# Optimization experiments

Measured on AMD Instinct MI355X. Metric: run time of the kernel, lower is better.

The kernel has to match this reference:

```python
import jax, jax.numpy as jnp
import numpy as np

N = 50000   # n_nodes (== input_dim, featureless identity features)
E = 800000  # edges per support (avg degree 16)
D = 200     # embed_dim (hardcoded in GIN)
C = 10      # num_classes


def setup_inputs() -> dict:
    key = jax.random.key(0)
    ks = jax.random.split(key, 8)
    x = jnp.zeros((N, 1), jnp.float32)  # unused: layer 0 is featureless
    rows0 = jax.random.randint(ks[0], (E,), 0, N, dtype=jnp.int32)
    cols0 = jax.random.randint(ks[1], (E,), 0, N, dtype=jnp.int32)
    vals0 = jax.random.uniform(ks[2], (E,), jnp.float32)
    rows1 = jax.random.randint(ks[3], (E,), 0, N, dtype=jnp.int32)
    cols1 = jax.random.randint(ks[4], (E,), 0, N, dtype=jnp.int32)
    vals1 = jax.random.uniform(ks[5], (E,), jnp.float32)
    W0 = jax.random.normal(ks[6], (N, D), jnp.float32) * 0.02
    W1 = jax.random.normal(ks[7], (D, C), jnp.float32) * 0.05
    eps0 = jnp.zeros((1,), jnp.float32)  # train_eps init (~1e-4 in repo)
    eps1 = jnp.zeros((1,), jnp.float32)
    return dict(x=x, rows0=rows0, cols0=cols0, vals0=vals0,
                rows1=rows1, cols1=cols1, vals1=vals1,
                W0=W0, W1=W1, eps0=eps0, eps1=eps1)


def reference(x, rows0, cols0, vals0, rows1, cols1, vals1, W0, W1, eps0, eps1):
    # sparse A @ X via gather + segment-sum (A in COO: rows, cols, vals)
    def spmm(r, c, v, X):
        return jax.ops.segment_sum(v[:, None] * X[c], r, num_segments=N)

    # Layer 0 (featureless, num_mlp_layers==1):
    #   AX = sum_i A_i ; out = AX @ W0 + 0.1*(1+eps0)*W0
    h0 = spmm(rows0, cols0, vals0, W0) + spmm(rows1, cols1, vals1, W0) \
         + 0.1 * (1.0 + eps0[0]) * W0
    h = jax.nn.relu(h0)  # [N, D]

    # Layer 1 (with features): out = (sum_i A_i @ h + 0.1*(1+eps1)*h) @ W1
    ax = spmm(rows0, cols0, vals0, h) + spmm(rows1, cols1, vals1, h)
    out = (ax + 0.1 * (1.0 + eps1[0]) * h) @ W1  # [N, C]
    return out
```

## Files before the change

### kernel.cpp

```cpp
#include <hip/hip_runtime.h>

#define N_NODES 50000
#define E_EDGES 800000
#define E2      (2 * E_EDGES)
#define D_DIM   200
#define C_CLS   10
#define NB_BUCKET 196
#define BATCH     4096
#define NB_SCATTER ((E2 + BATCH - 1) / BATCH)
#define NB_CONV    ((N_NODES * D_DIM / 4 + 255) / 256)
#define CAP       12288

static __device__ __forceinline__ unsigned f2bf(float f) {
    unsigned u = __float_as_uint(f);
    return (u + 0x7FFFu + ((u >> 16) & 1u)) >> 16;
}
static __device__ __forceinline__ float bf_lo(unsigned u) {
    return __uint_as_float(u << 16);
}
static __device__ __forceinline__ float bf_hi(unsigned u) {
    return __uint_as_float(u & 0xFFFF0000u);
}

__global__ __launch_bounds__(256) void convert_scatter_kernel(
        const float* __restrict__ W0, unsigned short* __restrict__ W0h,
        const int* __restrict__ rows0, const int* __restrict__ cols0,
        const float* __restrict__ vals0,
        const int* __restrict__ rows1, const int* __restrict__ cols1,
        const float* __restrict__ vals1,
        int* __restrict__ bcur,
        int2* __restrict__ stage) {
    __shared__ int cntL[NB_BUCKET];
    __shared__ int baseL[NB_BUCKET];
    __shared__ int offL[NB_BUCKET];
    __shared__ int2 recL[BATCH];

    if (blockIdx.x >= NB_SCATTER) {
        int i = ((blockIdx.x - NB_SCATTER) * 256 + threadIdx.x) * 4;
        if (i < N_NODES * D_DIM) {
            float4 f = *(const float4*)(W0 + i);
            uint2 p;
            p.x = f2bf(f.x) | (f2bf(f.y) << 16);
            p.y = f2bf(f.z) | (f2bf(f.w) << 16);
            *(uint2*)(W0h + i) = p;
        }
        return;
    }

    const int tid = threadIdx.x;
    const int e0 = blockIdx.x * BATCH;

    for (int b = tid; b < NB_BUCKET; b += 256) cntL[b] = 0;
    __syncthreads();

#pragma unroll
    for (int k = 0; k < BATCH / 256; ++k) {
        int idx = k * 256 + tid;
        int e = e0 + idx;
        if (e < E2) {
            int r, c;
            float v;
            if (e < E_EDGES) {
                r = rows0[e]; c = cols0[e]; v = vals0[e];
            } else {
                int e1 = e - E_EDGES;
                r = rows1[e1]; c = cols1[e1]; v = vals1[e1];
            }
            recL[idx] = make_int2((int)((unsigned)r | ((unsigned)c << 16)),
                                  __float_as_int(v));
            atomicAdd(&cntL[r >> 8], 1);
        }
    }
    __syncthreads();

    for (int b = tid; b < NB_BUCKET; b += 256) {
        int c = cntL[b];
        baseL[b] = (c > 0) ? atomicAdd(&bcur[b], c) : 0;
        offL[b] = 0;
    }
    __syncthreads();

#pragma unroll
    for (int k = 0; k < BATCH / 256; ++k) {
        int idx = k * 256 + tid;
        int e = e0 + idx;
        if (e < E2) {
            int2 rec = recL[idx];
            int b = (int)(((unsigned)rec.x & 0xFFFFu) >> 8);
            int pos = baseL[b] + atomicAdd(&offL[b], 1);
            stage[(size_t)b * CAP + pos] = rec;
        }
    }
}

__global__ __launch_bounds__(256) void build_csr_kernel(
        const int* __restrict__ bcur,
        const int2* __restrict__ stage,
        int* __restrict__ ticket,
        int2* __restrict__ rowseg,
        unsigned* __restrict__ cv4) {
    __shared__ int hist[256];
    __shared__ int lcur[256];
    __shared__ int ws4[4];
    __shared__ int sbase;
    const int b = blockIdx.x;
    const int tid = threadIdx.x;
    const int lane = tid & 63;
    const int w = tid >> 6;
    hist[tid] = 0;
    __syncthreads();

    const int n = bcur[b];
    const int2* __restrict__ sp = stage + (size_t)b * CAP;
    for (int i = tid; i < n; i += 256)
        atomicAdd(&hist[(unsigned)sp[i].x & 255u], 1);
    __syncthreads();

    int v = hist[tid];
    const int orig = v;
#pragma unroll
    for (int off = 1; off < 64; off <<= 1) {
        int t = __shfl_up(v, off, 64);
        if (lane >= off) v += t;
    }
    if (lane == 63) ws4[w] = v;
    __syncthreads();
    if (tid == 0) {
        int s = 0;
#pragma unroll
        for (int k = 0; k < 4; ++k) { int t = ws4[k]; ws4[k] = s; s += t; }
    }
    __syncthreads();
    v += ws4[w];

    if (tid == 255) sbase = atomicAdd(ticket, v);
    __syncthreads();

    const int start = sbase + v - orig;
    const int row = (b << 8) + tid;
    if (row < N_NODES) rowseg[row] = make_int2(start, orig);
    lcur[tid] = start;
    __syncthreads();

    for (int i = tid; i < n; i += 256) {
        int2 rec = sp[i];
        unsigned u = (unsigned)rec.x;
        int pos = atomicAdd(&lcur[u & 255u], 1);
        cv4[pos] = (u & 0xFFFF0000u) | f2bf(__int_as_float(rec.y));
    }
}

__global__ __launch_bounds__(256) void spmm_layer0_fused_kernel(
        const int2* __restrict__ rowseg,
        const unsigned* __restrict__ cv4,
        const unsigned short* __restrict__ W0h,
        const float* __restrict__ W1,
        const float* __restrict__ eps0,
        float* __restrict__ g) {
    __shared__ float W1s[D_DIM * C_CLS];
    for (int i = threadIdx.x; i < D_DIM * C_CLS; i += blockDim.x) W1s[i] = W1[i];
    __syncthreads();

    const int lane = threadIdx.x & 63;
    const int n = __builtin_amdgcn_readfirstlane(blockIdx.x * 4 + (threadIdx.x >> 6));
    if (n >= N_NODES) return;
    const float s0 = 0.1f * (1.0f + eps0[0]);
    const bool act = (lane < 50);
    const uint2* __restrict__ F = (const uint2*)W0h;

    const int2 seg = rowseg[n];
    const int beg  = seg.x;
    const int endp = seg.x + seg.y;
    float a0 = 0.f, a1 = 0.f, a2 = 0.f, a3 = 0.f;

    int e = beg;
    for (; e + 8 <= endp; e += 8) {
        unsigned w0 = cv4[e],     w1 = cv4[e + 1], w2 = cv4[e + 2], w3 = cv4[e + 3];
        unsigned w4 = cv4[e + 4], w5 = cv4[e + 5], w6 = cv4[e + 6], w7 = cv4[e + 7];
        if (act) {
            uint2 u0 = F[(size_t)(w0 >> 16) * 50 + lane];
            uint2 u1 = F[(size_t)(w1 >> 16) * 50 + lane];
            uint2 u2 = F[(size_t)(w2 >> 16) * 50 + lane];
            uint2 u3 = F[(size_t)(w3 >> 16) * 50 + lane];
            uint2 u4 = F[(size_t)(w4 >> 16) * 50 + lane];
            uint2 u5 = F[(size_t)(w5 >> 16) * 50 + lane];
            uint2 u6 = F[(size_t)(w6 >> 16) * 50 + lane];
            uint2 u7 = F[(size_t)(w7 >> 16) * 50 + lane];
            float v0 = __uint_as_float(w0 << 16), v1 = __uint_as_float(w1 << 16);
            float v2 = __uint_as_float(w2 << 16), v3 = __uint_as_float(w3 << 16);
            float v4 = __uint_as_float(w4 << 16), v5 = __uint_as_float(w5 << 16);
            float v6 = __uint_as_float(w6 << 16), v7 = __uint_as_float(w7 << 16);
            a0 += v0 * bf_lo(u0.x) + v1 * bf_lo(u1.x) + v2 * bf_lo(u2.x) + v3 * bf_lo(u3.x)
                + v4 * bf_lo(u4.x) + v5 * bf_lo(u5.x) + v6 * bf_lo(u6.x) + v7 * bf_lo(u7.x);
            a1 += v0 * bf_hi(u0.x) + v1 * bf_hi(u1.x) + v2 * bf_hi(u2.x) + v3 * bf_hi(u3.x)
                + v4 * bf_hi(u4.x) + v5 * bf_hi(u5.x) + v6 * bf_hi(u6.x) + v7 * bf_hi(u7.x);
            a2 += v0 * bf_lo(u0.y) + v1 * bf_lo(u1.y) + v2 * bf_lo(u2.y) + v3 * bf_lo(u3.y)
                + v4 * bf_lo(u4.y) + v5 * bf_lo(u5.y) + v6 * bf_lo(u6.y) + v7 * bf_lo(u7.y);
            a3 += v0 * bf_hi(u0.y) + v1 * bf_hi(u1.y) + v2 * bf_hi(u2.y) + v3 * bf_hi(u3.y)
                + v4 * bf_hi(u4.y) + v5 * bf_hi(u5.y) + v6 * bf_hi(u6.y) + v7 * bf_hi(u7.y);
        }
    }
    for (; e + 4 <= endp; e += 4) {
        unsigned w0 = cv4[e], w1 = cv4[e + 1], w2 = cv4[e + 2], w3 = cv4[e + 3];
        if (act) {
            uint2 u0 = F[(size_t)(w0 >> 16) * 50 + lane];
            uint2 u1 = F[(size_t)(w1 >> 16) * 50 + lane];
            uint2 u2 = F[(size_t)(w2 >> 16) * 50 + lane];
            uint2 u3 = F[(size_t)(w3 >> 16) * 50 + lane];
            float v0 = __uint_as_float(w0 << 16), v1 = __uint_as_float(w1 << 16);
            float v2 = __uint_as_float(w2 << 16), v3 = __uint_as_float(w3 << 16);
            a0 += v0 * bf_lo(u0.x) + v1 * bf_lo(u1.x) + v2 * bf_lo(u2.x) + v3 * bf_lo(u3.x);
            a1 += v0 * bf_hi(u0.x) + v1 * bf_hi(u1.x) + v2 * bf_hi(u2.x) + v3 * bf_hi(u3.x);
            a2 += v0 * bf_lo(u0.y) + v1 * bf_lo(u1.y) + v2 * bf_lo(u2.y) + v3 * bf_lo(u3.y);
            a3 += v0 * bf_hi(u0.y) + v1 * bf_hi(u1.y) + v2 * bf_hi(u2.y) + v3 * bf_hi(u3.y);
        }
    }
    for (; e < endp; ++e) {
        unsigned w = cv4[e];
        if (act) {
            uint2 u = F[(size_t)(w >> 16) * 50 + lane];
            float v = __uint_as_float(w << 16);
            a0 += v * bf_lo(u.x);
            a1 += v * bf_hi(u.x);
            a2 += v * bf_lo(u.y);
            a3 += v * bf_hi(u.y);
        }
    }

    float o[C_CLS];
#pragma unroll
    for (int k = 0; k < C_CLS; ++k) o[k] = 0.f;

    if (act) {
        uint2 w = F[(size_t)n * 50 + lane];
        a0 = fmaxf(a0 + s0 * bf_lo(w.x), 0.f);
        a1 = fmaxf(a1 + s0 * bf_hi(w.x), 0.f);
        a2 = fmaxf(a2 + s0 * bf_lo(w.y), 0.f);
        a3 = fmaxf(a3 + s0 * bf_hi(w.y), 0.f);
        const int d = lane * 4;
#pragma unroll
        for (int k = 0; k < C_CLS; ++k) {
            o[k] = a0 * W1s[(d + 0) * C_CLS + k]
                 + a1 * W1s[(d + 1) * C_CLS + k]
                 + a2 * W1s[(d + 2) * C_CLS + k]
                 + a3 * W1s[(d + 3) * C_CLS + k];
        }
    }

#pragma unroll
    for (int k = 0; k < C_CLS; ++k) {
        for (int off = 32; off > 0; off >>= 1)
            o[k] += __shfl_xor(o[k], off, 64);
    }

    if (lane == 0) {
        float* gp = g + (size_t)n * C_CLS;
#pragma unroll
        for (int k = 0; k < C_CLS; ++k) gp[k] = o[k];
    }
}

__global__ __launch_bounds__(256) void spmm_layer1_light_kernel(
        const int2* __restrict__ rowseg,
        const unsigned* __restrict__ cv4,
        const float* __restrict__ g,
        const float* __restrict__ eps1,
        float* __restrict__ out) {
    const int lane = threadIdx.x & 63;
    const int n = __builtin_amdgcn_readfirstlane(blockIdx.x * 4 + (threadIdx.x >> 6));
    if (n >= N_NODES) return;
    const int grp = lane / 10;
    const int d   = lane - grp * 10;
    const float s1 = 0.1f * (1.0f + eps1[0]);

    const int2 seg = rowseg[n];
    const int beg  = seg.x;
    const int endp = seg.x + seg.y;
    float acc = 0.f;

    for (int base = beg; base < endp; base += 12) {
        if (grp < 6) {
            int ea = base + grp;
            int eb = base + 6 + grp;
            unsigned pa = (ea < endp) ? cv4[ea] : 0u;
            unsigned pb = (eb < endp) ? cv4[eb] : 0u;
            if (ea < endp)
                acc += __uint_as_float(pa << 16) * g[(size_t)(pa >> 16) * C_CLS + d];
            if (eb < endp)
                acc += __uint_as_float(pb << 16) * g[(size_t)(pb >> 16) * C_CLS + d];
        }
    }

    float t;
    t = __shfl(acc, lane + 10, 64); if (lane < 50) acc += t;
    t = __shfl(acc, lane + 20, 64); if (lane < 30) acc += t;
    t = __shfl(acc, lane + 40, 64); if (lane < 10) acc += t;

    if (lane < 10) {
        out[(size_t)n * C_CLS + d] = acc + s1 * g[(size_t)n * C_CLS + d];
    }
}

extern "C" void kernel_launch(void* const* d_in, const int* in_sizes, int n_in,
                              void* d_out, int out_size, void* d_ws, size_t ws_size,
                              hipStream_t stream) {
    const int*   rows0 = (const int*)d_in[1];
    const int*   cols0 = (const int*)d_in[2];
    const float* vals0 = (const float*)d_in[3];
    const int*   rows1 = (const int*)d_in[4];
    const int*   cols1 = (const int*)d_in[5];
    const float* vals1 = (const float*)d_in[6];
    const float* W0    = (const float*)d_in[7];
    const float* W1    = (const float*)d_in[8];
    const float* eps0  = (const float*)d_in[9];
    const float* eps1  = (const float*)d_in[10];
    float* out = (float*)d_out;

    char* ws = (char*)d_ws;
    size_t off = 0;
    auto alloc = [&](size_t bytes) {
        void* p = ws + off;
        off += (bytes + 255) & ~(size_t)255;
        return p;
    };
    unsigned short* W0h = (unsigned short*)alloc((size_t)N_NODES * D_DIM * 2);
    float* g      = (float*)alloc((size_t)N_NODES * C_CLS * 4);
    int2* rowseg  = (int2*)alloc((size_t)N_NODES * 8);
    int* bcur     = (int*)alloc((size_t)(NB_BUCKET + 1) * 4);
    unsigned* cv4 = (unsigned*)alloc((size_t)E2 * 4);
    int2* stage   = (int2*)alloc((size_t)NB_BUCKET * CAP * 8);
    int* ticket   = bcur + NB_BUCKET;
    (void)ws_size;

    hipMemsetAsync(bcur, 0, (size_t)(NB_BUCKET + 1) * 4, stream);
    convert_scatter_kernel<<<NB_SCATTER + NB_CONV, 256, 0, stream>>>(
        W0, W0h, rows0, cols0, vals0, rows1, cols1, vals1, bcur, stage);
    build_csr_kernel<<<NB_BUCKET, 256, 0, stream>>>(bcur, stage, ticket, rowseg, cv4);

    const int spmm_grid = (N_NODES + 3) / 4;
    spmm_layer0_fused_kernel<<<spmm_grid, 256, 0, stream>>>(
        rowseg, cv4, W0h, W1, eps0, g);
    spmm_layer1_light_kernel<<<spmm_grid, 256, 0, stream>>>(
        rowseg, cv4, g, eps1, out);
}
```

Before: 273.8 us.

## Sort edges locally in LDS before coalesced scatter and CSR writeback

The scatter kernel now counts bucket sizes first, prefix-sums them, and places each record into a bucket-sorted LDS array. It then writes contiguous runs to the global stage buffer, finding each position's bucket by binary search. The CSR build kernel likewise assembles its column/value entries in a 48KB LDS buffer and copies them out contiguously. Both changes target scattered, uncoalesced global writes. The cost is reading the edge arrays twice, extra LDS use that may reduce occupancy, and a binary search per record.

```diff
diff --git a/kernel.cpp b/kernel.cpp
--- a/kernel.cpp
+++ b/kernel.cpp
@@ -30,10 +30,12 @@
         const float* __restrict__ vals1,
         int* __restrict__ bcur,
         int2* __restrict__ stage) {
-    __shared__ int cntL[NB_BUCKET];
-    __shared__ int baseL[NB_BUCKET];
-    __shared__ int offL[NB_BUCKET];
-    __shared__ int2 recL[BATCH];
+    __shared__ int cntL[256];
+    __shared__ int lofs[256];
+    __shared__ int baseG[NB_BUCKET];
+    __shared__ int cur[NB_BUCKET];
+    __shared__ int ws4[4];
+    __shared__ int2 recL2[BATCH];
 
     if (blockIdx.x >= NB_SCATTER) {
         int i = ((blockIdx.x - NB_SCATTER) * 256 + threadIdx.x) * 4;
@@ -48,35 +50,47 @@
     }
 
     const int tid = threadIdx.x;
+    const int lane = tid & 63;
+    const int w = tid >> 6;
     const int e0 = blockIdx.x * BATCH;
-
-    for (int b = tid; b < NB_BUCKET; b += 256) cntL[b] = 0;
+    const int m = min(BATCH, E2 - e0);
+
+    cntL[tid] = 0;
     __syncthreads();
 
 #pragma unroll
     for (int k = 0; k < BATCH / 256; ++k) {
         int idx = k * 256 + tid;
         int e = e0 + idx;
-        if (e < E2) {
-            int r, c;
-            float v;
-            if (e < E_EDGES) {
-                r = rows0[e]; c = cols0[e]; v = vals0[e];
-            } else {
-                int e1 = e - E_EDGES;
-                r = rows1[e1]; c = cols1[e1]; v = vals1[e1];
-            }
-            recL[idx] = make_int2((int)((unsigned)r | ((unsigned)c << 16)),
-                                  __float_as_int(v));
+        if (idx < m) {
+            int r = (e < E_EDGES) ? rows0[e] : rows1[e - E_EDGES];
             atomicAdd(&cntL[r >> 8], 1);
         }
     }
     __syncthreads();
 
-    for (int b = tid; b < NB_BUCKET; b += 256) {
-        int c = cntL[b];
-        baseL[b] = (c > 0) ? atomicAdd(&bcur[b], c) : 0;
-        offL[b] = 0;
+    int v = cntL[tid];
+    const int orig = v;
+#pragma unroll
+    for (int off = 1; off < 64; off <<= 1) {
+        int t = __shfl_up(v, off, 64);
+        if (lane >= off) v += t;
+    }
+    if (lane == 63) ws4[w] = v;
+    __syncthreads();
+    if (tid == 0) {
+        int s = 0;
+#pragma unroll
+        for (int k = 0; k < 4; ++k) { int t = ws4[k]; ws4[k] = s; s += t; }
+    }
+    __syncthreads();
+    lofs[tid] = v + ws4[w] - orig;
+    __syncthreads();
+
+    if (tid < NB_BUCKET) {
+        int c = cntL[tid];
+        baseG[tid] = (c > 0) ? atomicAdd(&bcur[tid], c) : 0;
+        cur[tid] = lofs[tid];
     }
     __syncthreads();
 
@@ -84,12 +98,29 @@
     for (int k = 0; k < BATCH / 256; ++k) {
         int idx = k * 256 + tid;
         int e = e0 + idx;
-        if (e < E2) {
-            int2 rec = recL[idx];
-            int b = (int)(((unsigned)rec.x & 0xFFFFu) >> 8);
-            int pos = baseL[b] + atomicAdd(&offL[b], 1);
-            stage[(size_t)b * CAP + pos] = rec;
-        }
+        if (idx < m) {
+            int r, c;
+            float val;
+            if (e < E_EDGES) {
+                r = rows0[e]; c = cols0[e]; val = vals0[e];
+            } else {
+                int e1 = e - E_EDGES;
+                r = rows1[e1]; c = cols1[e1]; val = vals1[e1];
+            }
+            int p = atomicAdd(&cur[r >> 8], 1);
+            recL2[p] = make_int2((int)((unsigned)r | ((unsigned)c << 16)),
+                                 __float_as_int(val));
+        }
+    }
+    __syncthreads();
+
+    for (int p = tid; p < m; p += 256) {
+        int lo = 0, hi = NB_BUCKET - 1;
+        while (lo < hi) {
+            int mid = (lo + hi + 1) >> 1;
+            if (lofs[mid] <= p) lo = mid; else hi = mid - 1;
+        }
+        stage[(size_t)lo * CAP + baseG[lo] + (p - lofs[lo])] = recL2[p];
     }
 }
 
@@ -103,6 +134,8 @@
     __shared__ int lcur[256];
     __shared__ int ws4[4];
     __shared__ int sbase;
+    __shared__ int stot;
+    __shared__ unsigned cv4L[CAP];
     const int b = blockIdx.x;
     const int tid = threadIdx.x;
     const int lane = tid & 63;
@@ -133,21 +166,27 @@
     __syncthreads();
     v += ws4[w];
 
-    if (tid == 255) sbase = atomicAdd(ticket, v);
-    __syncthreads();
-
-    const int start = sbase + v - orig;
+    if (tid == 255) {
+        stot = v;
+        sbase = atomicAdd(ticket, v);
+    }
+    __syncthreads();
+
     const int row = (b << 8) + tid;
-    if (row < N_NODES) rowseg[row] = make_int2(start, orig);
-    lcur[tid] = start;
+    if (row < N_NODES) rowseg[row] = make_int2(sbase + v - orig, orig);
+    lcur[tid] = v - orig;
     __syncthreads();
 
     for (int i = tid; i < n; i += 256) {
         int2 rec = sp[i];
         unsigned u = (unsigned)rec.x;
         int pos = atomicAdd(&lcur[u & 255u], 1);
-        cv4[pos] = (u & 0xFFFF0000u) | f2bf(__int_as_float(rec.y));
-    }
+        cv4L[pos] = (u & 0xFFFF0000u) | f2bf(__int_as_float(rec.y));
+    }
+    __syncthreads();
+
+    for (int i = tid; i < stot; i += 256)
+        cv4[sbase + i] = cv4L[i];
 }
 
 __global__ __launch_bounds__(256) void spmm_layer0_fused_kernel(
```

After: 276.9 us. No clear change (+1.1%).
